# Optimization experiments

Measured on AMD Instinct MI355X. Metric: run time of the kernel, lower is better.

The kernel has to match this reference:

```python
import jax, jax.numpy as jnp
import numpy as np
import math

D_IN = 4096
D_OUT = 4096
RANK = 8
SCALE = 16.0 / 8.0  # alpha / rank


def fwht(x):
    """Fast Walsh-Hadamard transform over last dim (power of two), orthonormal."""
    d = x.shape[-1]
    orig_shape = x.shape
    h = 1
    while h < d:
        y = x.reshape(x.shape[:-1] + (d // (2 * h), 2, h))
        a = y[..., 0, :]
        b = y[..., 1, :]
        x = jnp.stack([a + b, a - b], axis=-2).reshape(orig_shape)
        h <<= 1
    return x / math.sqrt(d)


def srht_right_multiply(x, signs, perm):
    # x @ P  (sign flip -> column permutation -> FWHT)
    return fwht((x * signs)[..., perm])


def srht_right_multiply_T(x, signs, inv_perm):
    # x @ P^T (FWHT -> inverse permutation -> sign flip)
    return fwht(x)[..., inv_perm] * signs


def setup_inputs() -> dict:
    key = jax.random.key(0)
    ks = jax.random.split(key, 10)
    x = jax.random.normal(ks[0], (4, 2048, D_IN), dtype=jnp.float32)
    W = jax.random.normal(ks[1], (D_OUT, D_IN), dtype=jnp.float32) * 0.02
    b = jax.random.normal(ks[2], (D_OUT,), dtype=jnp.float32) * 0.02
    # kaiming-uniform-ish init for A; random B (real module zero-inits B, but
    # random B exercises the full adapter path for correctness checking)
    bound = 1.0 / math.sqrt(D_IN)
    A = jax.random.uniform(ks[3], (RANK, D_IN), minval=-bound, maxval=bound, dtype=jnp.float32)
    B = jax.random.normal(ks[4], (D_OUT, RANK), dtype=jnp.float32) * 0.02
    in_signs = (jax.random.randint(ks[5], (D_IN,), 0, 2) * 2 - 1).astype(jnp.float32)
    out_signs = (jax.random.randint(ks[6], (D_OUT,), 0, 2) * 2 - 1).astype(jnp.float32)
    in_perm = jax.random.permutation(ks[7], D_IN).astype(jnp.int32)
    in_inv_perm = jnp.argsort(in_perm).astype(jnp.int32)
    out_perm = jax.random.permutation(ks[8], D_OUT).astype(jnp.int32)
    out_inv_perm = jnp.argsort(out_perm).astype(jnp.int32)
    return {
        "x": x, "W": W, "b": b, "A": A, "B": B,
        "in_signs": in_signs, "out_signs": out_signs,
        "in_perm": in_perm, "in_inv_perm": in_inv_perm,
        "out_perm": out_perm, "out_inv_perm": out_inv_perm,
    }


def reference(x, W, b, A, B, in_signs, out_signs, in_perm, in_inv_perm, out_perm, out_inv_perm):
    # base linear
    residual = jnp.einsum('bsi,oi->bso', x, W) + b
    # adapter path: x @ P_in^T @ A^T @ B^T @ P_out, scaled
    adapter_in = srht_right_multiply_T(x, in_signs, in_inv_perm)  # [b,s,in]
    down = jnp.einsum('bsi,ri->bsr', adapter_in, A)               # [b,s,rank]
    up = jnp.einsum('bsr,or->bso', down, B)                       # [b,s,out]
    up = srht_right_multiply(up, out_signs, out_perm)
    return residual + SCALE * up
```

## Files before the change

### kernel.cpp

```cpp
#include <hip/hip_runtime.h>
#include <stdint.h>
#include <stddef.h>

#define DDIM 4096
#define MROWS 8192
#define RANK 8

typedef __attribute__((ext_vector_type(8))) short bf16x8;
typedef __attribute__((ext_vector_type(4))) float f32x4;
typedef __attribute__((ext_vector_type(4))) unsigned short u16x4;

__device__ __forceinline__ unsigned short f2bf(float f) {
  union { float f; unsigned int u; } c; c.f = f;
  unsigned int u = c.u + 0x7fffu + ((c.u >> 16) & 1u);
  return (unsigned short)(u >> 16);
}

__global__ void convert_x_kernel(const float4* __restrict__ x, u16x4* __restrict__ out) {
  int idx = blockIdx.x * 256 + threadIdx.x;
  float4 v = x[idx];
  u16x4 o;
  o.x = f2bf(v.x); o.y = f2bf(v.y); o.z = f2bf(v.z); o.w = f2bf(v.w);
  out[idx] = o;
}

__global__ void srht_fold_kernel(const float* __restrict__ A, const float* __restrict__ Bm,
                                 const float* __restrict__ in_signs,
                                 const float* __restrict__ out_signs,
                                 const int* __restrict__ in_perm,
                                 const int* __restrict__ out_perm,
                                 float* __restrict__ A2, float* __restrict__ B2t) {
  __shared__ float buf[DDIM];
  const int tid = threadIdx.x;
  const int b = blockIdx.x;
  if (b < RANK) {
    const int r = b;
    for (int j = tid; j < DDIM; j += 256) {
      int p = in_perm[j];
      buf[j] = in_signs[p] * A[r * DDIM + p];
    }
  } else {
    const int r = b - RANK;
    for (int j = tid; j < DDIM; j += 256) {
      int p = out_perm[j];
      buf[j] = out_signs[p] * Bm[p * RANK + r];
    }
  }
  __syncthreads();
  for (int h = 1; h < DDIM; h <<= 1) {
    for (int p = tid; p < DDIM / 2; p += 256) {
      int j = p & (h - 1);
      int i0 = ((p - j) << 1) + j;
      int i1 = i0 + h;
      float a = buf[i0], c = buf[i1];
      buf[i0] = a + c;
      buf[i1] = a - c;
    }
    __syncthreads();
  }
  const float scale = (b < RANK) ? (1.0f / 64.0f) : (2.0f / 64.0f);
  float* dst = (b < RANK) ? (A2 + b * DDIM) : (B2t + (b - RANK) * DDIM);
  for (int j = tid; j < DDIM; j += 256) dst[j] = buf[j] * scale;
}

__global__ void weff_kernel(const float4* __restrict__ W, const float* __restrict__ A2,
                            const float* __restrict__ B2t, u16x4* __restrict__ Weff) {
  int idx = blockIdx.x * 256 + threadIdx.x;
  int o = idx >> 10;
  int ci = idx & 1023;
  float4 w = W[idx];
#pragma unroll
  for (int r = 0; r < RANK; ++r) {
    float s = B2t[r * DDIM + o];
    float4 a = ((const float4*)(A2 + r * DDIM))[ci];
    w.x += s * a.x; w.y += s * a.y; w.z += s * a.z; w.w += s * a.w;
  }
  u16x4 u;
  u.x = f2bf(w.x); u.y = f2bf(w.y); u.z = f2bf(w.z); u.w = f2bf(w.w);
  Weff[idx] = u;
}

__device__ __forceinline__ void async_copy16(const unsigned short* g, unsigned short* l) {
  __builtin_amdgcn_global_load_lds(
      (const __attribute__((address_space(1))) unsigned int*)g,
      (__attribute__((address_space(3))) unsigned int*)l, 16, 0, 0);
}

__global__ __launch_bounds__(256) void gemm_bt_kernel(
    const unsigned short* __restrict__ Ab,
    const unsigned short* __restrict__ Bb,
    const float* __restrict__ bias,
    float* __restrict__ C) {
  constexpr int K = 4096, N = 4096;
  __shared__ unsigned short As[128 * 64];
  __shared__ unsigned short Bs[128 * 64];

  const int tid = threadIdx.x;
  const int pid = blockIdx.x;

  const int GRID_N = 32;
  const int grpsz = 8 * GRID_N;
  const int group = pid / grpsz;
  const int lpid = pid % grpsz;
  const int m_blk = group * 8 + (lpid & 7);
  const int n_blk = lpid >> 3;

  const int mBase = m_blk * 128;
  const int nBase = n_blk * 128;

  const int sr = tid >> 3;
  const int sc = (tid & 7) ^ (sr & 7);
  const unsigned short* ga[4];
  const unsigned short* gb[4];
#pragma unroll
  for (int j = 0; j < 4; ++j) {
    ga[j] = Ab + (size_t)(mBase + j * 32 + sr) * K + sc * 8;
    gb[j] = Bb + (size_t)(nBase + j * 32 + sr) * K + sc * 8;
  }
  unsigned short* lA = As + tid * 8;
  unsigned short* lB = Bs + tid * 8;

  const int lane = tid & 63;
  const int wid = tid >> 6;
  const int wm = wid >> 1;
  const int wn = wid & 1;
  const int lrow = lane & 15;
  const int quad = lane >> 4;

  int aoff[4][2], boff[4][2];
#pragma unroll
  for (int mt = 0; mt < 4; ++mt) {
    int r = wm * 64 + mt * 16 + lrow;
#pragma unroll
    for (int ks = 0; ks < 2; ++ks) {
      int c = ks * 4 + quad;
      aoff[mt][ks] = r * 64 + ((c ^ (r & 7)) * 8);
    }
  }
#pragma unroll
  for (int nt = 0; nt < 4; ++nt) {
    int r = wn * 64 + nt * 16 + lrow;
#pragma unroll
    for (int ks = 0; ks < 2; ++ks) {
      int c = ks * 4 + quad;
      boff[nt][ks] = r * 64 + ((c ^ (r & 7)) * 8);
    }
  }

  f32x4 acc[4][4];
#pragma unroll
  for (int mt = 0; mt < 4; ++mt)
#pragma unroll
    for (int nt = 0; nt < 4; ++nt)
      acc[mt][nt] = (f32x4){0.f, 0.f, 0.f, 0.f};

  for (int kt = 0; kt < K / 64; ++kt) {
#pragma unroll
    for (int j = 0; j < 4; ++j) async_copy16(ga[j], lA + j * 2048);
#pragma unroll
    for (int j = 0; j < 4; ++j) async_copy16(gb[j], lB + j * 2048);
#pragma unroll
    for (int j = 0; j < 4; ++j) { ga[j] += 64; gb[j] += 64; }
    __syncthreads();
#pragma unroll
    for (int ks = 0; ks < 2; ++ks) {
      bf16x8 af[4], bfr[4];
#pragma unroll
      for (int mt = 0; mt < 4; ++mt) af[mt] = *(const bf16x8*)(As + aoff[mt][ks]);
#pragma unroll
      for (int nt = 0; nt < 4; ++nt) bfr[nt] = *(const bf16x8*)(Bs + boff[nt][ks]);
#pragma unroll
      for (int mt = 0; mt < 4; ++mt)
#pragma unroll
        for (int nt = 0; nt < 4; ++nt)
          acc[mt][nt] = __builtin_amdgcn_mfma_f32_16x16x32_bf16(af[mt], bfr[nt],
                                                                acc[mt][nt], 0, 0, 0);
    }
    __syncthreads();
  }

#pragma unroll
  for (int nt = 0; nt < 4; ++nt) {
    const int col = nBase + wn * 64 + nt * 16 + lrow;
    const float bc = bias[col];
#pragma unroll
    for (int mt = 0; mt < 4; ++mt) {
      const int row0 = mBase + wm * 64 + mt * 16 + quad * 4;
      float* cp = C + (size_t)row0 * N + col;
#pragma unroll
      for (int i = 0; i < 4; ++i)
        cp[(size_t)i * N] = acc[mt][nt][i] + bc;
    }
  }
}

extern "C" void kernel_launch(void* const* d_in, const int* in_sizes, int n_in,
                              void* d_out, int out_size, void* d_ws, size_t ws_size,
                              hipStream_t stream) {
  const float* x        = (const float*)d_in[0];
  const float* W        = (const float*)d_in[1];
  const float* b        = (const float*)d_in[2];
  const float* A        = (const float*)d_in[3];
  const float* Bm       = (const float*)d_in[4];
  const float* in_signs = (const float*)d_in[5];
  const float* out_signs= (const float*)d_in[6];
  const int*   in_perm  = (const int*)d_in[7];
  const int*   out_perm = (const int*)d_in[9];
  float* out = (float*)d_out;

  char* ws = (char*)d_ws;
  unsigned short* x_bf = (unsigned short*)ws;
  unsigned short* weff = (unsigned short*)(ws + (size_t)67108864);
  float* A2  = (float*)(ws + (size_t)67108864 + (size_t)33554432);
  float* B2t = A2 + RANK * DDIM;

  convert_x_kernel<<<32768, 256, 0, stream>>>((const float4*)x, (u16x4*)x_bf);
  srht_fold_kernel<<<16, 256, 0, stream>>>(A, Bm, in_signs, out_signs, in_perm, out_perm,
                                           A2, B2t);
  weff_kernel<<<16384, 256, 0, stream>>>((const float4*)W, A2, B2t, (u16x4*)weff);
  gemm_bt_kernel<<<2048, 256, 0, stream>>>(x_bf, weff, b, out);
}
```

Measured before the change: 659.4 us.

## Switch GEMM to 32x32x16 MFMA and widen conversion kernels to 8 elements

The GEMM inner loop moves from 16x16x32 to 32x32x16 bf16 MFMA, with 2x2 fragments per wave in place of 4x4. This cuts the number of LDS fragment loads and MFMA issues per tile, and the epilogue is rewritten for the 32x32 accumulator layout. The x-conversion and W-fold kernels each process 8 elements per thread so they can write 16-byte stores, and the SRHT fold kernel uses 1024 threads per block. The epilogue stores remain column-strided and scattered.

Measured after the change: 609.5 us. 7.6% less time.

```diff
diff --git a/kernel.cpp b/kernel.cpp
--- a/kernel.cpp
+++ b/kernel.cpp
@@ -8,7 +8,9 @@
 
 typedef __attribute__((ext_vector_type(8))) short bf16x8;
 typedef __attribute__((ext_vector_type(4))) float f32x4;
+typedef __attribute__((ext_vector_type(16))) float f32x16;
 typedef __attribute__((ext_vector_type(4))) unsigned short u16x4;
+typedef __attribute__((ext_vector_type(8))) unsigned short u16x8;
 
 __device__ __forceinline__ unsigned short f2bf(float f) {
   union { float f; unsigned int u; } c; c.f = f;
@@ -16,39 +18,40 @@
   return (unsigned short)(u >> 16);
 }
 
-__global__ void convert_x_kernel(const float4* __restrict__ x, u16x4* __restrict__ out) {
+__global__ void convert_x_kernel(const float4* __restrict__ x, u16x8* __restrict__ out) {
   int idx = blockIdx.x * 256 + threadIdx.x;
-  float4 v = x[idx];
-  u16x4 o;
-  o.x = f2bf(v.x); o.y = f2bf(v.y); o.z = f2bf(v.z); o.w = f2bf(v.w);
+  float4 v0 = x[2 * idx];
+  float4 v1 = x[2 * idx + 1];
+  u16x8 o;
+  o[0] = f2bf(v0.x); o[1] = f2bf(v0.y); o[2] = f2bf(v0.z); o[3] = f2bf(v0.w);
+  o[4] = f2bf(v1.x); o[5] = f2bf(v1.y); o[6] = f2bf(v1.z); o[7] = f2bf(v1.w);
   out[idx] = o;
 }
 
-__global__ void srht_fold_kernel(const float* __restrict__ A, const float* __restrict__ Bm,
-                                 const float* __restrict__ in_signs,
-                                 const float* __restrict__ out_signs,
-                                 const int* __restrict__ in_perm,
-                                 const int* __restrict__ out_perm,
-                                 float* __restrict__ A2, float* __restrict__ B2t) {
+__global__ __launch_bounds__(1024) void srht_fold_kernel(
+    const float* __restrict__ A, const float* __restrict__ Bm,
+    const float* __restrict__ in_signs, const float* __restrict__ out_signs,
+    const int* __restrict__ in_perm, const int* __restrict__ out_perm,
+    float* __restrict__ A2, float* __restrict__ B2t) {
   __shared__ float buf[DDIM];
   const int tid = threadIdx.x;
   const int b = blockIdx.x;
   if (b < RANK) {
     const int r = b;
-    for (int j = tid; j < DDIM; j += 256) {
+    for (int j = tid; j < DDIM; j += 1024) {
       int p = in_perm[j];
       buf[j] = in_signs[p] * A[r * DDIM + p];
     }
   } else {
     const int r = b - RANK;
-    for (int j = tid; j < DDIM; j += 256) {
+    for (int j = tid; j < DDIM; j += 1024) {
       int p = out_perm[j];
       buf[j] = out_signs[p] * Bm[p * RANK + r];
     }
   }
   __syncthreads();
   for (int h = 1; h < DDIM; h <<= 1) {
-    for (int p = tid; p < DDIM / 2; p += 256) {
+    for (int p = tid; p < DDIM / 2; p += 1024) {
       int j = p & (h - 1);
       int i0 = ((p - j) << 1) + j;
       int i1 = i0 + h;
@@ -60,23 +63,27 @@
   }
   const float scale = (b < RANK) ? (1.0f / 64.0f) : (2.0f / 64.0f);
   float* dst = (b < RANK) ? (A2 + b * DDIM) : (B2t + (b - RANK) * DDIM);
-  for (int j = tid; j < DDIM; j += 256) dst[j] = buf[j] * scale;
+  for (int j = tid; j < DDIM; j += 1024) dst[j] = buf[j] * scale;
 }
 
 __global__ void weff_kernel(const float4* __restrict__ W, const float* __restrict__ A2,
-                            const float* __restrict__ B2t, u16x4* __restrict__ Weff) {
+                            const float* __restrict__ B2t, u16x8* __restrict__ Weff) {
   int idx = blockIdx.x * 256 + threadIdx.x;
-  int o = idx >> 10;
-  int ci = idx & 1023;
-  float4 w = W[idx];
+  int o = idx >> 9;
+  int c8 = idx & 511;
+  float4 w0 = W[2 * idx];
+  float4 w1 = W[2 * idx + 1];
 #pragma unroll
   for (int r = 0; r < RANK; ++r) {
     float s = B2t[r * DDIM + o];
-    float4 a = ((const float4*)(A2 + r * DDIM))[ci];
-    w.x += s * a.x; w.y += s * a.y; w.z += s * a.z; w.w += s * a.w;
-  }
-  u16x4 u;
-  u.x = f2bf(w.x); u.y = f2bf(w.y); u.z = f2bf(w.z); u.w = f2bf(w.w);
+    const float4* av = (const float4*)(A2 + r * DDIM) + 2 * c8;
+    float4 a0 = av[0], a1 = av[1];
+    w0.x += s * a0.x; w0.y += s * a0.y; w0.z += s * a0.z; w0.w += s * a0.w;
+    w1.x += s * a1.x; w1.y += s * a1.y; w1.z += s * a1.z; w1.w += s * a1.w;
+  }
+  u16x8 u;
+  u[0] = f2bf(w0.x); u[1] = f2bf(w0.y); u[2] = f2bf(w0.z); u[3] = f2bf(w0.w);
+  u[4] = f2bf(w1.x); u[5] = f2bf(w1.y); u[6] = f2bf(w1.z); u[7] = f2bf(w1.w);
   Weff[idx] = u;
 }
 
@@ -124,35 +131,36 @@
   const int wid = tid >> 6;
   const int wm = wid >> 1;
   const int wn = wid & 1;
-  const int lrow = lane & 15;
-  const int quad = lane >> 4;
-
-  int aoff[4][2], boff[4][2];
-#pragma unroll
-  for (int mt = 0; mt < 4; ++mt) {
-    int r = wm * 64 + mt * 16 + lrow;
-#pragma unroll
-    for (int ks = 0; ks < 2; ++ks) {
-      int c = ks * 4 + quad;
+  const int lm = lane & 31;
+  const int half = lane >> 5;
+
+  int aoff[2][4], boff[2][4];
+#pragma unroll
+  for (int mt = 0; mt < 2; ++mt) {
+    int r = wm * 64 + mt * 32 + lm;
+#pragma unroll
+    for (int ks = 0; ks < 4; ++ks) {
+      int c = ks * 2 + half;
       aoff[mt][ks] = r * 64 + ((c ^ (r & 7)) * 8);
     }
   }
 #pragma unroll
-  for (int nt = 0; nt < 4; ++nt) {
-    int r = wn * 64 + nt * 16 + lrow;
-#pragma unroll
-    for (int ks = 0; ks < 2; ++ks) {
-      int c = ks * 4 + quad;
+  for (int nt = 0; nt < 2; ++nt) {
+    int r = wn * 64 + nt * 32 + lm;
+#pragma unroll
+    for (int ks = 0; ks < 4; ++ks) {
+      int c = ks * 2 + half;
       boff[nt][ks] = r * 64 + ((c ^ (r & 7)) * 8);
     }
   }
 
-  f32x4 acc[4][4];
-#pragma unroll
-  for (int mt = 0; mt < 4; ++mt)
-#pragma unroll
-    for (int nt = 0; nt < 4; ++nt)
-      acc[mt][nt] = (f32x4){0.f, 0.f, 0.f, 0.f};
+  f32x16 acc[2][2];
+#pragma unroll
+  for (int mt = 0; mt < 2; ++mt)
+#pragma unroll
+    for (int nt = 0; nt < 2; ++nt)
+#pragma unroll
+      for (int i = 0; i < 16; ++i) acc[mt][nt][i] = 0.f;
 
   for (int kt = 0; kt < K / 64; ++kt) {
 #pragma unroll
@@ -163,33 +171,35 @@
     for (int j = 0; j < 4; ++j) { ga[j] += 64; gb[j] += 64; }
     __syncthreads();
 #pragma unroll
-    for (int ks = 0; ks < 2; ++ks) {
-      bf16x8 af[4], bfr[4];
-#pragma unroll
-      for (int mt = 0; mt < 4; ++mt) af[mt] = *(const bf16x8*)(As + aoff[mt][ks]);
-#pragma unroll
-      for (int nt = 0; nt < 4; ++nt) bfr[nt] = *(const bf16x8*)(Bs + boff[nt][ks]);
-#pragma unroll
-      for (int mt = 0; mt < 4; ++mt)
-#pragma unroll
-        for (int nt = 0; nt < 4; ++nt)
-          acc[mt][nt] = __builtin_amdgcn_mfma_f32_16x16x32_bf16(af[mt], bfr[nt],
+    for (int ks = 0; ks < 4; ++ks) {
+      bf16x8 af[2], bfr[2];
+#pragma unroll
+      for (int mt = 0; mt < 2; ++mt) af[mt] = *(const bf16x8*)(As + aoff[mt][ks]);
+#pragma unroll
+      for (int nt = 0; nt < 2; ++nt) bfr[nt] = *(const bf16x8*)(Bs + boff[nt][ks]);
+#pragma unroll
+      for (int mt = 0; mt < 2; ++mt)
+#pragma unroll
+        for (int nt = 0; nt < 2; ++nt)
+          acc[mt][nt] = __builtin_amdgcn_mfma_f32_32x32x16_bf16(af[mt], bfr[nt],
                                                                 acc[mt][nt], 0, 0, 0);
     }
     __syncthreads();
   }
 
 #pragma unroll
-  for (int nt = 0; nt < 4; ++nt) {
-    const int col = nBase + wn * 64 + nt * 16 + lrow;
+  for (int nt = 0; nt < 2; ++nt) {
+    const int col = nBase + wn * 64 + nt * 32 + lm;
     const float bc = bias[col];
 #pragma unroll
-    for (int mt = 0; mt < 4; ++mt) {
-      const int row0 = mBase + wm * 64 + mt * 16 + quad * 4;
+    for (int mt = 0; mt < 2; ++mt) {
+      const int row0 = mBase + wm * 64 + mt * 32 + 4 * half;
       float* cp = C + (size_t)row0 * N + col;
 #pragma unroll
-      for (int i = 0; i < 4; ++i)
-        cp[(size_t)i * N] = acc[mt][nt][i] + bc;
+      for (int reg = 0; reg < 16; ++reg) {
+        int row = (reg & 3) + 8 * (reg >> 2);
+        cp[(size_t)row * N] = acc[mt][nt][reg] + bc;
+      }
     }
   }
 }
@@ -214,9 +224,9 @@
   float* A2  = (float*)(ws + (size_t)67108864 + (size_t)33554432);
   float* B2t = A2 + RANK * DDIM;
 
-  convert_x_kernel<<<32768, 256, 0, stream>>>((const float4*)x, (u16x4*)x_bf);
-  srht_fold_kernel<<<16, 256, 0, stream>>>(A, Bm, in_signs, out_signs, in_perm, out_perm,
-                                           A2, B2t);
-  weff_kernel<<<16384, 256, 0, stream>>>((const float4*)W, A2, B2t, (u16x4*)weff);
+  convert_x_kernel<<<16384, 256, 0, stream>>>((const float4*)x, (u16x8*)x_bf);
+  srht_fold_kernel<<<16, 1024, 0, stream>>>(A, Bm, in_signs, out_signs, in_perm, out_perm,
+                                            A2, B2t);
+  weff_kernel<<<8192, 256, 0, stream>>>((const float4*)W, A2, B2t, (u16x8*)weff);
   gemm_bt_kernel<<<2048, 256, 0, stream>>>(x_bf, weff, b, out);
 }
```
